# Kernel tuning notes

Hardware: AMD Instinct MI355X
Metric: run time of the kernel (lower is better)

The kernel has to match this reference:

```python
import jax, jax.numpy as jnp
import numpy as np

DIM = 512
HIDDEN = 512
HEADS = 8
HEAD_DIM = HIDDEN // HEADS
SCALE = HEAD_DIM ** -0.5
B, H, W = 2, 64, 64


def setup_inputs() -> dict:
    key = jax.random.key(0)
    ks = jax.random.split(key, 12)
    init = lambda k, shp: jax.random.normal(k, shp, dtype=jnp.float32) * 0.02
    return {
        "x": jax.random.normal(ks[0], (B, DIM, H, W), dtype=jnp.float32),
        "context": jax.random.normal(ks[1], (B, DIM, H, W), dtype=jnp.float32),
        # weights stored [in, out] so y = x @ W + b
        "Wi": init(ks[2], (DIM, HIDDEN)), "bi": jnp.zeros((HIDDEN,), jnp.float32),
        "Wc": init(ks[3], (DIM, HIDDEN)), "bc": jnp.zeros((HIDDEN,), jnp.float32),
        "Wq": init(ks[4], (HIDDEN, HIDDEN)),
        "Wk": init(ks[5], (HIDDEN, HIDDEN)),
        "Wv": init(ks[6], (HIDDEN, HIDDEN)),
        "Wo1": init(ks[7], (HIDDEN, HIDDEN)), "bo1": jnp.zeros((HIDDEN,), jnp.float32),
        "Wo2": init(ks[8], (HIDDEN, DIM)), "bo2": jnp.zeros((DIM,), jnp.float32),
    }


def reference(x, context, Wi, bi, Wc, bc, Wq, Wk, Wv, Wo1, bo1, Wo2, bo2):
    b, c, h, w = x.shape
    s = h * w
    x_seq = x.reshape(b, c, s).transpose(0, 2, 1)        # [B,S,C]
    ctx_seq = context.reshape(b, c, s).transpose(0, 2, 1)

    x_proj = x_seq @ Wi + bi                              # [B,S,Hid]
    ctx_proj = ctx_seq @ Wc + bc

    q = (x_proj @ Wq).reshape(b, s, HEADS, HEAD_DIM)      # [B,S,h,d]
    k = (ctx_proj @ Wk).reshape(b, s, HEADS, HEAD_DIM)
    v = (ctx_proj @ Wv).reshape(b, s, HEADS, HEAD_DIM)

    attn = jnp.einsum('bqhd,bkhd->bhqk', q, k) * SCALE    # [B,h,S,S]
    attn = jax.nn.softmax(attn, axis=-1)
    out = jnp.einsum('bhqk,bkhd->bqhd', attn, v).reshape(b, s, HIDDEN)

    out = jax.nn.gelu(out @ Wo1 + bo1, approximate=False) @ Wo2 + bo2  # [B,S,C]
    return out.transpose(0, 2, 1).reshape(b, c, h, w)
```

## Files before the change

kernel.cpp:

```cpp
#include <hip/hip_runtime.h>

#define SEQ 4096
#define CDIM 512
#define HID 512
#define NB 2
#define NHEADS 8

typedef float f32x4 __attribute__((ext_vector_type(4)));
typedef short bf16x8 __attribute__((ext_vector_type(8)));

static __device__ __forceinline__ short f2bf(float f) {
  unsigned u = __float_as_uint(f);
  u = (u + 0x7fffu + ((u >> 16) & 1u)) >> 16;
  return (short)u;
}
static __device__ __forceinline__ float bf2f(short h) {
  return __uint_as_float(((unsigned)(unsigned short)h) << 16);
}
static __device__ __forceinline__ unsigned pk2bf(float a, float b) {
  unsigned r;
  asm("v_cvt_pk_bf16_f32 %0, %1, %2" : "=v"(r) : "v"(a), "v"(b));
  return r;
}
typedef const __attribute__((address_space(1))) char gas_char;
typedef __attribute__((address_space(3))) char las_char;
static __device__ __forceinline__ void gll16(const char* g, char* l) {
  __builtin_amdgcn_global_load_lds((gas_char*)g, (las_char*)l, 16, 0, 0);
}

__global__ __launch_bounds__(256) void prep_w(
    const float* Wi, const float* Wc, const float* Wq, const float* Wk,
    const float* Wv, const float* Wo1, const float* Wo2,
    unsigned short* wth, unsigned short* wtl) {
  __shared__ float tile[32][33];
  const int z = blockIdx.z;
  const float* src;
  float scale = 1.0f;
  switch (z) {
    case 0: src = Wi; break;
    case 1: src = Wc; break;
    case 2: src = Wq; scale = 0.18033688011112042f; break;
    case 3: src = Wk; break;
    case 4: src = Wv; break;
    case 5: src = Wo1; break;
    default: src = Wo2; break;
  }
  const int n0 = blockIdx.x * 32, k0 = blockIdx.y * 32;
  const int tx = threadIdx.x, ty = threadIdx.y;
  for (int i = ty; i < 32; i += 8)
    tile[i][tx] = src[(k0 + i) * 512 + n0 + tx];
  __syncthreads();
  unsigned short* oh = wth + z * 262144;
  unsigned short* ol = wtl + z * 262144;
  if (z < 2) {
    for (int i = ty; i < 32; i += 8) {
      const float v = tile[i][tx];
      const short h = f2bf(v);
      oh[(k0 + i) * 512 + n0 + tx] = (unsigned short)h;
      ol[(k0 + i) * 512 + n0 + tx] = (unsigned short)f2bf(v - bf2f(h));
    }
  } else {
    for (int i = ty; i < 32; i += 8) {
      const float v = tile[tx][i] * scale;
      const short h = f2bf(v);
      oh[(n0 + i) * 512 + k0 + tx] = (unsigned short)h;
      ol[(n0 + i) * 512 + k0 + tx] = (unsigned short)f2bf(v - bf2f(h));
    }
  }
}

__global__ __launch_bounds__(512) void prep_bias(
    const float* __restrict__ bi, const float* __restrict__ Wq,
    const float* __restrict__ bc, const float* __restrict__ Wk,
    const float* __restrict__ Wv, float* __restrict__ bout) {
  const int z = blockIdx.x;
  const int n = threadIdx.x;
  const float* b = (z == 0) ? bi : bc;
  const float* W = (z == 0) ? Wq : (z == 1) ? Wk : Wv;
  const float s = (z == 0) ? 0.18033688011112042f : 1.0f;
  float acc = 0.0f;
  for (int k = 0; k < 512; ++k) acc += b[k] * W[k * 512 + n];
  bout[z * 512 + n] = acc * s;
}

__global__ __launch_bounds__(256) void prep_x2(
    const float* __restrict__ x, const float* __restrict__ ctx,
    unsigned short* __restrict__ oh0, unsigned short* __restrict__ ol0,
    unsigned short* __restrict__ oh1, unsigned short* __restrict__ ol1) {
  __shared__ float tile[32][33];
  const int b = blockIdx.z & 1;
  const int ten = blockIdx.z >> 1;
  const float* in = ten ? ctx : x;
  unsigned short* oh = ten ? oh1 : oh0;
  unsigned short* ol = ten ? ol1 : ol0;
  const int s0 = blockIdx.x * 32, c0 = blockIdx.y * 32;
  const int tx = threadIdx.x, ty = threadIdx.y;
  const float* ib = in + (long)b * CDIM * SEQ;
  for (int i = ty; i < 32; i += 8)
    tile[i][tx] = ib[(long)(c0 + i) * SEQ + s0 + tx];
  __syncthreads();
  const long ob = (long)b * SEQ * CDIM;
  for (int i = ty; i < 32; i += 8) {
    const float v = tile[tx][i];
    const short h = f2bf(v);
    oh[ob + (long)(s0 + i) * CDIM + c0 + tx] = (unsigned short)h;
    ol[ob + (long)(s0 + i) * CDIM + c0 + tx] = (unsigned short)f2bf(v - bf2f(h));
  }
}

#define OUT_DUAL 0
#define OUT_HI 1
#define OUT_F32 2

struct GemmJob {
  const unsigned short *Ah, *Al, *Wh, *Wl;
  const float* bias;
  void *outA, *outB;
  int tstore;
};

template <int OMODE, bool DO_GELU, bool HASB, int NJOBS, int GY, int NBATCH>
__global__ __launch_bounds__(256) void gemmN(GemmJob J0, GemmJob J1, GemmJob J2) {
  __shared__ __align__(16) char lds[49152];
  const int orig = blockIdx.x + ((blockIdx.y + blockIdx.z * GY) << 3);
  const int total = 8 * GY * NBATCH * NJOBS;
  const int work = (orig & 7) * (total >> 3) + (orig >> 3);
  const int bx = work & 7;
  const int rest = work >> 3;
  const int by = rest % GY;
  const int z = rest / GY;
  const int jz = z / NBATCH;
  const int bz = z % NBATCH;
  const GemmJob J = (NJOBS >= 3 && jz == 2) ? J2 : ((NJOBS >= 2 && jz == 1) ? J1 : J0);
  const int TS = J.tstore;
  const int t = threadIdx.x;
  const int lane = t & 63, wave = t >> 6;
  const int l15 = lane & 15, g = lane >> 4;
  const int m0 = by * 128, n0 = bx * 64;
  const long abase = (long)bz * SEQ * 512;

  const int grow = lane >> 3;
  const int ch = (((lane & 7) << 4) ^ (grow << 4));
  const int chp = ch & 63;
  const char* pa = (const char*)((ch < 64) ? J.Ah : J.Al);
  const char* pw = (const char*)((ch < 64) ? J.Wh : J.Wl);
  const char* aG[4];
#pragma unroll
  for (int i = 0; i < 4; ++i)
    aG[i] = pa + ((abase + (long)(m0 + wave * 32 + i * 8 + grow) * 512) << 1) + chp;
  const char* wG[2];
#pragma unroll
  for (int i = 0; i < 2; ++i)
    wG[i] = pw + (((long)(n0 + wave * 16 + i * 8 + grow) * 512) << 1) + chp;

  f32x4 acc[4][2];
#pragma unroll
  for (int p = 0; p < 4; ++p)
#pragma unroll
    for (int q = 0; q < 2; ++q) acc[p][q] = (f32x4){0.f, 0.f, 0.f, 0.f};

  {
    char* LA = lds;
    char* LW = lds + 16384;
#pragma unroll
    for (int i = 0; i < 4; ++i) gll16(aG[i], LA + wave * 4096 + i * 1024);
#pragma unroll
    for (int i = 0; i < 2; ++i) gll16(wG[i], LW + wave * 2048 + i * 1024);
  }

  int buf = 0;
  for (int k0 = 0; k0 < 512; k0 += 32) {
    char* LA = lds + buf * 24576;
    char* LW = LA + 16384;
    __syncthreads();
    if (k0 + 32 < 512) {
      char* NA = lds + (buf ^ 1) * 24576;
      char* NW = NA + 16384;
      const int koff = (k0 + 32) * 2;
#pragma unroll
      for (int i = 0; i < 4; ++i) gll16(aG[i] + koff, NA + wave * 4096 + i * 1024);
#pragma unroll
      for (int i = 0; i < 2; ++i) gll16(wG[i] + koff, NW + wave * 2048 + i * 1024);
    }

    if (!TS) {
      bf16x8 fbh[2], fbl[2];
#pragma unroll
      for (int q = 0; q < 2; ++q) {
        const int r = wave * 32 + q * 16 + l15;
        const char* rp = LA + r * 128;
        const int sw = (r & 7) << 4;
        fbh[q] = *(const bf16x8*)(rp + ((g << 4) ^ sw));
        fbl[q] = *(const bf16x8*)(rp + (((4 + g) << 4) ^ sw));
      }
#pragma unroll
      for (int p = 0; p < 4; ++p) {
        const int r = p * 16 + l15;
        const char* rp = LW + r * 128;
        const int sw = (r & 7) << 4;
        const bf16x8 fah = *(const bf16x8*)(rp + ((g << 4) ^ sw));
        const bf16x8 fal = *(const bf16x8*)(rp + (((4 + g) << 4) ^ sw));
#pragma unroll
        for (int q = 0; q < 2; ++q) {
          acc[p][q] = __builtin_amdgcn_mfma_f32_16x16x32_bf16(fah, fbh[q], acc[p][q], 0, 0, 0);
          acc[p][q] = __builtin_amdgcn_mfma_f32_16x16x32_bf16(fah, fbl[q], acc[p][q], 0, 0, 0);
          acc[p][q] = __builtin_amdgcn_mfma_f32_16x16x32_bf16(fal, fbh[q], acc[p][q], 0, 0, 0);
        }
      }
    } else {
      const int mB = (wave >> 1) * 64, nB = (wave & 1) * 32;
      bf16x8 fbh[2], fbl[2];
#pragma unroll
      for (int q = 0; q < 2; ++q) {
        const int r = nB + q * 16 + l15;
        const char* rp = LW + r * 128;
        const int sw = (r & 7) << 4;
        fbh[q] = *(const bf16x8*)(rp + ((g << 4) ^ sw));
        fbl[q] = *(const bf16x8*)(rp + (((4 + g) << 4) ^ sw));
      }
#pragma unroll
      for (int p = 0; p < 4; ++p) {
        const int r = mB + p * 16 + l15;
        const char* rp = LA + r * 128;
        const int sw = (r & 7) << 4;
        const bf16x8 fah = *(const bf16x8*)(rp + ((g << 4) ^ sw));
        const bf16x8 fal = *(const bf16x8*)(rp + (((4 + g) << 4) ^ sw));
#pragma unroll
        for (int q = 0; q < 2; ++q) {
          acc[p][q] = __builtin_amdgcn_mfma_f32_16x16x32_bf16(fah, fbh[q], acc[p][q], 0, 0, 0);
          acc[p][q] = __builtin_amdgcn_mfma_f32_16x16x32_bf16(fah, fbl[q], acc[p][q], 0, 0, 0);
          acc[p][q] = __builtin_amdgcn_mfma_f32_16x16x32_bf16(fal, fbh[q], acc[p][q], 0, 0, 0);
        }
      }
    }
    buf ^= 1;
  }

  const long obase = (long)bz * 512 * SEQ;
#pragma unroll
  for (int p = 0; p < 4; ++p)
#pragma unroll
    for (int q = 0; q < 2; ++q) {
      f32x4 v = acc[p][q];
      if (TS) {
        const int m = m0 + (wave >> 1) * 64 + p * 16 + 4 * g;
        const int n = n0 + (wave & 1) * 32 + q * 16 + l15;
        if (HASB) {
          const float b = J.bias[n];
          v[0] += b; v[1] += b; v[2] += b; v[3] += b;
        }
        if (OMODE == OUT_F32) {
          float4 f;
          f.x = v[0]; f.y = v[1]; f.z = v[2]; f.w = v[3];
          *(float4*)((float*)J.outA + obase + (long)n * SEQ + m) = f;
        } else {
          const short4 h4 = make_short4(f2bf(v[0]), f2bf(v[1]), f2bf(v[2]), f2bf(v[3]));
          *(short4*)((unsigned short*)J.outA + obase + (long)n * SEQ + m) = h4;
        }
      } else {
        const int n = n0 + p * 16 + 4 * g;
        const int m = m0 + wave * 32 + q * 16 + l15;
        if (HASB) v += *(const f32x4*)(J.bias + n);
        if (DO_GELU) {
#pragma unroll
          for (int r = 0; r < 4; ++r)
            v[r] = 0.5f * v[r] * (1.0f + erff(v[r] * 0.7071067811865476f));
        }
        unsigned short* oA = (unsigned short*)J.outA + obase + (long)m * 512 + n;
        if (OMODE == OUT_DUAL) {
          short h[4], l[4];
#pragma unroll
          for (int r = 0; r < 4; ++r) {
            h[r] = f2bf(v[r]);
            l[r] = f2bf(v[r] - bf2f(h[r]));
          }
          *(short4*)oA = make_short4(h[0], h[1], h[2], h[3]);
          *(short4*)((unsigned short*)J.outB + obase + (long)m * 512 + n) =
              make_short4(l[0], l[1], l[2], l[3]);
        } else {
          *(short4*)oA = make_short4(f2bf(v[0]), f2bf(v[1]), f2bf(v[2]), f2bf(v[3]));
        }
      }
    }
}

__global__ __launch_bounds__(512) void attn_mfma(
    const unsigned short* __restrict__ qh, const unsigned short* __restrict__ kh,
    const unsigned short* __restrict__ vt, unsigned short* __restrict__ oh,
    unsigned short* __restrict__ ol) {
  __shared__ __align__(16) char smem[32768];
  const int t = threadIdx.x;
  const int lane = t & 63;
  const int wave = t >> 6;
  const int l15 = lane & 15;
  const int g = lane >> 4;
  const int orig = blockIdx.x + ((blockIdx.y + (blockIdx.z << 3)) << 4);
  const int work = ((orig & 7) << 5) + (orig >> 3);
  const int hd = (work >> 4) & 7;
  const int bz = work >> 7;
  const int q0 = (work & 15) * 256;
  const long sbase = (long)bz * SEQ * 512;
  const long tbase = (long)bz * 512 * SEQ;

  const int grow = lane >> 3;
  const int ch = (((lane & 7) << 4) ^ (grow << 4));
  const char* kG = (const char*)kh + (sbase << 1) + hd * 128 +
                   (long)(wave * 8 + grow) * 1024 + ch;
  const char* vG = (const char*)vt +
                   ((tbase + (long)(hd * 64 + wave * 8 + grow) * 4096) << 1) + ch;

  const int swzl = (l15 & 7) << 4;
  const int kfb = l15 * 128 + g * 16;
  const int vfb = l15 * 128 + g * 8;

  bf16x8 qf[2][2];
#pragma unroll
  for (int u = 0; u < 2; ++u) {
    const unsigned short* qrow =
        qh + sbase + (long)(q0 + wave * 32 + u * 16 + l15) * 512 + hd * 64 + g * 8;
    qf[u][0] = *(const bf16x8*)(qrow);
    qf[u][1] = *(const bf16x8*)(qrow + 32);
  }

  bf16x8 vones;
#pragma unroll
  for (int e = 0; e < 8; ++e) vones[e] = (l15 == 0) ? (short)0x3f80 : (short)0;

  f32x4 acc[2][4];
  f32x4 acc5[2];
#pragma unroll
  for (int u = 0; u < 2; ++u) {
    acc5[u] = (f32x4){0.f, 0.f, 0.f, 0.f};
#pragma unroll
    for (int dt = 0; dt < 4; ++dt) acc[u][dt] = (f32x4){0.f, 0.f, 0.f, 0.f};
  }

  gll16(kG, smem + wave * 1024);
  gll16(vG, smem + 8192 + wave * 1024);

  int buf = 0;
  for (int j0 = 0; j0 < SEQ; j0 += 64) {
    char* Kl = smem + buf * 16384;
    char* Vl = Kl + 8192;
    __syncthreads();
    if (j0 + 64 < SEQ) {
      char* Kn = smem + (buf ^ 1) * 16384;
      gll16(kG + (long)(j0 + 64) * 1024, Kn + wave * 1024);
      gll16(vG + (long)(j0 + 64) * 2, Kn + 8192 + wave * 1024);
    }

    f32x4 st[2][4];
    __builtin_amdgcn_s_setprio(1);
#pragma unroll
    for (int kt = 0; kt < 4; ++kt) {
      const bf16x8 ka0 = *(const bf16x8*)(Kl + ((kt * 2048 + kfb) ^ swzl));
      const bf16x8 ka1 = *(const bf16x8*)(Kl + ((kt * 2048 + kfb + 64) ^ swzl));
      f32x4 s0 = {0.f, 0.f, 0.f, 0.f};
      f32x4 s1 = {0.f, 0.f, 0.f, 0.f};
      s0 = __builtin_amdgcn_mfma_f32_16x16x32_bf16(ka0, qf[0][0], s0, 0, 0, 0);
      s0 = __builtin_amdgcn_mfma_f32_16x16x32_bf16(ka1, qf[0][1], s0, 0, 0, 0);
      s1 = __builtin_amdgcn_mfma_f32_16x16x32_bf16(ka0, qf[1][0], s1, 0, 0, 0);
      s1 = __builtin_amdgcn_mfma_f32_16x16x32_bf16(ka1, qf[1][1], s1, 0, 0, 0);
      st[0][kt] = s0;
      st[1][kt] = s1;
    }
    __builtin_amdgcn_s_setprio(0);

    union Pb { bf16x8 v8; unsigned u4[4]; } pb[2][2];
#pragma unroll
    for (int u = 0; u < 2; ++u) {
#pragma unroll
      for (int kt = 0; kt < 4; ++kt)
#pragma unroll
        for (int r = 0; r < 4; ++r)
          st[u][kt][r] = __builtin_amdgcn_exp2f(st[u][kt][r]);
#pragma unroll
      for (int kc = 0; kc < 2; ++kc)
#pragma unroll
        for (int h = 0; h < 2; ++h) {
          pb[u][kc].u4[h * 2 + 0] = pk2bf(st[u][2 * kc + h][0], st[u][2 * kc + h][1]);
          pb[u][kc].u4[h * 2 + 1] = pk2bf(st[u][2 * kc + h][2], st[u][2 * kc + h][3]);
        }
    }

    __builtin_amdgcn_s_setprio(1);
#pragma unroll
    for (int dt = 0; dt < 4; ++dt) {
      union { bf16x8 v8; int2 h2[2]; } va0, va1;
      va0.h2[0] = *(const int2*)(Vl + ((dt * 2048 + vfb) ^ swzl));
      va0.h2[1] = *(const int2*)(Vl + ((dt * 2048 + vfb + 32) ^ swzl));
      va1.h2[0] = *(const int2*)(Vl + ((dt * 2048 + vfb + 64) ^ swzl));
      va1.h2[1] = *(const int2*)(Vl + ((dt * 2048 + vfb + 96) ^ swzl));
      acc[0][dt] = __builtin_amdgcn_mfma_f32_16x16x32_bf16(va0.v8, pb[0][0].v8, acc[0][dt], 0, 0, 0);
      acc[0][dt] = __builtin_amdgcn_mfma_f32_16x16x32_bf16(va1.v8, pb[0][1].v8, acc[0][dt], 0, 0, 0);
      acc[1][dt] = __builtin_amdgcn_mfma_f32_16x16x32_bf16(va0.v8, pb[1][0].v8, acc[1][dt], 0, 0, 0);
      acc[1][dt] = __builtin_amdgcn_mfma_f32_16x16x32_bf16(va1.v8, pb[1][1].v8, acc[1][dt], 0, 0, 0);
    }
#pragma unroll
    for (int u = 0; u < 2; ++u) {
      acc5[u] = __builtin_amdgcn_mfma_f32_16x16x32_bf16(vones, pb[u][0].v8, acc5[u], 0, 0, 0);
      acc5[u] = __builtin_amdgcn_mfma_f32_16x16x32_bf16(vones, pb[u][1].v8, acc5[u], 0, 0, 0);
    }
    __builtin_amdgcn_s_setprio(0);
    buf ^= 1;
  }

#pragma unroll
  for (int u = 0; u < 2; ++u) {
    const float lt = __shfl(acc5[u][0], l15);
    const float inv = 1.0f / lt;
    const long orow = sbase + (long)(q0 + wave * 32 + u * 16 + l15) * 512 + hd * 64;
#pragma unroll
    for (int dt = 0; dt < 4; ++dt) {
      short h[4], l[4];
#pragma unroll
      for (int r = 0; r < 4; ++r) {
        const float v = acc[u][dt][r] * inv;
        h[r] = f2bf(v);
        l[r] = f2bf(v - bf2f(h[r]));
      }
      *(short4*)(oh + orow + dt * 16 + g * 4) = make_short4(h[0], h[1], h[2], h[3]);
      *(short4*)(ol + orow + dt * 16 + g * 4) = make_short4(l[0], l[1], l[2], l[3]);
    }
  }
}

extern "C" void kernel_launch(void* const* d_in, const int* in_sizes, int n_in,
                              void* d_out, int out_size, void* d_ws,
                              size_t ws_size, hipStream_t stream) {
  const float* x   = (const float*)d_in[0];
  const float* ctx = (const float*)d_in[1];
  const float* Wi  = (const float*)d_in[2];
  const float* bi  = (const float*)d_in[3];
  const float* Wc  = (const float*)d_in[4];
  const float* bc  = (const float*)d_in[5];
  const float* Wq  = (const float*)d_in[6];
  const float* Wk  = (const float*)d_in[7];
  const float* Wv  = (const float*)d_in[8];
  const float* Wo1 = (const float*)d_in[9];
  const float* bo1 = (const float*)d_in[10];
  const float* Wo2 = (const float*)d_in[11];
  const float* bo2 = (const float*)d_in[12];
  float* out = (float*)d_out;

  const size_t WP = 262144;
  char* p = (char*)d_ws;
  unsigned short* wth = (unsigned short*)p; p += (size_t)7 * WP * 2;
  unsigned short* wtl = (unsigned short*)p; p += (size_t)7 * WP * 2;
  unsigned short* cwh = (unsigned short*)p; p += (size_t)3 * WP * 2;
  unsigned short* cwl = (unsigned short*)p; p += (size_t)3 * WP * 2;
  float* bqkv = (float*)p; p += 3 * 512 * 4;
  const size_t PLE = (size_t)NB * SEQ * 512;
  unsigned short* P1 = (unsigned short*)p; p += PLE * 2;
  unsigned short* P2 = (unsigned short*)p; p += PLE * 2;
  unsigned short* P3 = (unsigned short*)p; p += PLE * 2;
  unsigned short* P4 = (unsigned short*)p; p += PLE * 2;
  unsigned short* P5 = (unsigned short*)p; p += PLE * 2;
  unsigned short* P6 = (unsigned short*)p; p += PLE * 2;
  unsigned short* P7 = (unsigned short*)d_out;

  const dim3 gb(256);
  const dim3 pg(16, 16, 7), pbk(32, 8);
  const dim3 xg(128, 16, 2 * NB);
  GemmJob jn = {};

  prep_w<<<pg, pbk, 0, stream>>>(Wi, Wc, Wq, Wk, Wv, Wo1, Wo2, wth, wtl);
  prep_bias<<<dim3(3), dim3(512), 0, stream>>>(bi, Wq, bc, Wk, Wv, bqkv);
  prep_x2<<<xg, pbk, 0, stream>>>(x, ctx, P1, P2, P3, P4);
  {
    GemmJob ja = {wth + 2 * WP, wtl + 2 * WP, wth + 0 * WP, wtl + 0 * WP,
                  nullptr, cwh + 0 * WP, cwl + 0 * WP, 0};
    GemmJob jb = {wth + 3 * WP, wtl + 3 * WP, wth + 1 * WP, wtl + 1 * WP,
                  nullptr, cwh + 1 * WP, cwl + 1 * WP, 0};
    GemmJob jc = {wth + 4 * WP, wtl + 4 * WP, wth + 1 * WP, wtl + 1 * WP,
                  nullptr, cwh + 2 * WP, cwl + 2 * WP, 0};
    gemmN<OUT_DUAL, false, false, 3, 4, 1><<<dim3(8, 4, 3), gb, 0, stream>>>(ja, jb, jc);
  }
  {
    GemmJob ja = {P1, P2, cwh + 0 * WP, cwl + 0 * WP, bqkv + 0, P5, nullptr, 0};
    GemmJob jb = {P3, P4, cwh + 1 * WP, cwl + 1 * WP, bqkv + 512, P6, nullptr, 0};
    GemmJob jc = {P3, P4, cwh + 2 * WP, cwl + 2 * WP, bqkv + 1024, P7, nullptr, 1};
    gemmN<OUT_HI, false, true, 3, 32, 2><<<dim3(8, 32, 6), gb, 0, stream>>>(ja, jb, jc);
  }
  attn_mfma<<<dim3(SEQ / 256, NHEADS, NB), dim3(512), 0, stream>>>(P5, P6, P7, P1, P2);
  {
    GemmJob j = {P1, P2, wth + 5 * WP, wtl + 5 * WP, bo1, P3, P4, 0};
    gemmN<OUT_DUAL, true, true, 1, 32, 2><<<dim3(8, 32, 2), gb, 0, stream>>>(j, jn, jn);
  }
  {
    GemmJob j = {P3, P4, wth + 6 * WP, wtl + 6 * WP, bo2, out, nullptr, 1};
    gemmN<OUT_F32, false, true, 1, 32, 2><<<dim3(8, 32, 2), gb, 0, stream>>>(j, jn, jn);
  }
}
```

Before: 214.9 us.

## Triple-buffer GEMM and attention loads and drop a split-bf16 term for QKV

Measured after the change: 218.4 us. No clear change (+1.6%).

```diff
diff --git a/kernel.cpp b/kernel.cpp
--- a/kernel.cpp
+++ b/kernel.cpp
@@ -26,6 +26,11 @@
 typedef __attribute__((address_space(3))) char las_char;
 static __device__ __forceinline__ void gll16(const char* g, char* l) {
   __builtin_amdgcn_global_load_lds((gas_char*)g, (las_char*)l, 16, 0, 0);
+}
+#define WAITV(N) asm volatile("s_waitcnt vmcnt(" #N ")" ::: "memory")
+static __device__ __forceinline__ void pipe_barrier() {
+  __builtin_amdgcn_s_barrier();
+  __builtin_amdgcn_sched_barrier(0);
 }
 
 __global__ __launch_bounds__(256) void prep_w(
@@ -119,9 +124,9 @@
   int tstore;
 };
 
-template <int OMODE, bool DO_GELU, bool HASB, int NJOBS, int GY, int NBATCH>
+template <int OMODE, bool DO_GELU, bool HASB, int NJOBS, int GY, int NBATCH, int TERMS>
 __global__ __launch_bounds__(256) void gemmN(GemmJob J0, GemmJob J1, GemmJob J2) {
-  __shared__ __align__(16) char lds[49152];
+  __shared__ __align__(16) char lds[73728];
   const int orig = blockIdx.x + ((blockIdx.y + blockIdx.z * GY) << 3);
   const int total = 8 * GY * NBATCH * NJOBS;
   const int work = (orig & 7) * (total >> 3) + (orig >> 3);
@@ -153,35 +158,32 @@
   for (int i = 0; i < 2; ++i)
     wG[i] = pw + (((long)(n0 + wave * 16 + i * 8 + grow) * 512) << 1) + chp;
 
+  auto stage = [&](int tt, int b) {
+    char* LA = lds + b * 24576;
+    char* LW = LA + 16384;
+    const int koff = tt * 64;
+#pragma unroll
+    for (int i = 0; i < 4; ++i) gll16(aG[i] + koff, LA + wave * 4096 + i * 1024);
+    gll16(wG[0] + koff, LW + wave * 2048);
+    gll16(wG[1] + koff, LW + wave * 2048 + 1024);
+  };
+
   f32x4 acc[4][2];
 #pragma unroll
   for (int p = 0; p < 4; ++p)
 #pragma unroll
     for (int q = 0; q < 2; ++q) acc[p][q] = (f32x4){0.f, 0.f, 0.f, 0.f};
 
-  {
-    char* LA = lds;
-    char* LW = lds + 16384;
-#pragma unroll
-    for (int i = 0; i < 4; ++i) gll16(aG[i], LA + wave * 4096 + i * 1024);
-#pragma unroll
-    for (int i = 0; i < 2; ++i) gll16(wG[i], LW + wave * 2048 + i * 1024);
-  }
-
-  int buf = 0;
-  for (int k0 = 0; k0 < 512; k0 += 32) {
-    char* LA = lds + buf * 24576;
+  stage(0, 0);
+  stage(1, 1);
+
+  int it = 0;
+  for (int k0 = 0; k0 < 512; k0 += 32, ++it) {
+    if (k0 == 480) { WAITV(0); } else { WAITV(6); }
+    pipe_barrier();
+    if (k0 + 64 < 512) stage(it + 2, (it + 2) % 3);
+    char* LA = lds + (it % 3) * 24576;
     char* LW = LA + 16384;
-    __syncthreads();
-    if (k0 + 32 < 512) {
-      char* NA = lds + (buf ^ 1) * 24576;
-      char* NW = NA + 16384;
-      const int koff = (k0 + 32) * 2;
-#pragma unroll
-      for (int i = 0; i < 4; ++i) gll16(aG[i] + koff, NA + wave * 4096 + i * 1024);
-#pragma unroll
-      for (int i = 0; i < 2; ++i) gll16(wG[i] + koff, NW + wave * 2048 + i * 1024);
-    }
 
     if (!TS) {
       bf16x8 fbh[2], fbl[2];
@@ -199,12 +201,16 @@
         const char* rp = LW + r * 128;
         const int sw = (r & 7) << 4;
         const bf16x8 fah = *(const bf16x8*)(rp + ((g << 4) ^ sw));
-        const bf16x8 fal = *(const bf16x8*)(rp + (((4 + g) << 4) ^ sw));
 #pragma unroll
         for (int q = 0; q < 2; ++q) {
           acc[p][q] = __builtin_amdgcn_mfma_f32_16x16x32_bf16(fah, fbh[q], acc[p][q], 0, 0, 0);
           acc[p][q] = __builtin_amdgcn_mfma_f32_16x16x32_bf16(fah, fbl[q], acc[p][q], 0, 0, 0);
-          acc[p][q] = __builtin_amdgcn_mfma_f32_16x16x32_bf16(fal, fbh[q], acc[p][q], 0, 0, 0);
+        }
+        if (TERMS == 3) {
+          const bf16x8 fal = *(const bf16x8*)(rp + (((4 + g) << 4) ^ sw));
+#pragma unroll
+          for (int q = 0; q < 2; ++q)
+            acc[p][q] = __builtin_amdgcn_mfma_f32_16x16x32_bf16(fal, fbh[q], acc[p][q], 0, 0, 0);
         }
       }
     } else {
@@ -216,7 +222,7 @@
         const char* rp = LW + r * 128;
         const int sw = (r & 7) << 4;
         fbh[q] = *(const bf16x8*)(rp + ((g << 4) ^ sw));
-        fbl[q] = *(const bf16x8*)(rp + (((4 + g) << 4) ^ sw));
+        if (TERMS == 3) fbl[q] = *(const bf16x8*)(rp + (((4 + g) << 4) ^ sw));
       }
 #pragma unroll
       for (int p = 0; p < 4; ++p) {
@@ -228,12 +234,12 @@
 #pragma unroll
         for (int q = 0; q < 2; ++q) {
           acc[p][q] = __builtin_amdgcn_mfma_f32_16x16x32_bf16(fah, fbh[q], acc[p][q], 0, 0, 0);
-          acc[p][q] = __builtin_amdgcn_mfma_f32_16x16x32_bf16(fah, fbl[q], acc[p][q], 0, 0, 0);
+          if (TERMS == 3)
+            acc[p][q] = __builtin_amdgcn_mfma_f32_16x16x32_bf16(fah, fbl[q], acc[p][q], 0, 0, 0);
           acc[p][q] = __builtin_amdgcn_mfma_f32_16x16x32_bf16(fal, fbh[q], acc[p][q], 0, 0, 0);
         }
       }
     }
-    buf ^= 1;
   }
 
   const long obase = (long)bz * 512 * SEQ;
@@ -288,7 +294,7 @@
     const unsigned short* __restrict__ qh, const unsigned short* __restrict__ kh,
     const unsigned short* __restrict__ vt, unsigned short* __restrict__ oh,
     unsigned short* __restrict__ ol) {
-  __shared__ __align__(16) char smem[32768];
+  __shared__ __align__(16) char smem[49152];
   const int t = threadIdx.x;
   const int lane = t & 63;
   const int wave = t >> 6;
@@ -326,6 +332,12 @@
 #pragma unroll
   for (int e = 0; e < 8; ++e) vones[e] = (l15 == 0) ? (short)0x3f80 : (short)0;
 
+  auto stage = [&](int j0s, int b) {
+    char* Kn = smem + b * 16384;
+    gll16(kG + (long)j0s * 1024, Kn + wave * 1024);
+    gll16(vG + (long)j0s * 2, Kn + 8192 + wave * 1024);
+  };
+
   f32x4 acc[2][4];
   f32x4 acc5[2];
 #pragma unroll
@@ -335,19 +347,16 @@
     for (int dt = 0; dt < 4; ++dt) acc[u][dt] = (f32x4){0.f, 0.f, 0.f, 0.f};
   }
 
-  gll16(kG, smem + wave * 1024);
-  gll16(vG, smem + 8192 + wave * 1024);
-
-  int buf = 0;
-  for (int j0 = 0; j0 < SEQ; j0 += 64) {
-    char* Kl = smem + buf * 16384;
+  stage(0, 0);
+  stage(64, 1);
+
+  int it = 0;
+  for (int j0 = 0; j0 < SEQ; j0 += 64, ++it) {
+    if (j0 == SEQ - 64) { WAITV(0); } else { WAITV(2); }
+    pipe_barrier();
+    if (j0 + 128 < SEQ) stage(j0 + 128, (it + 2) % 3);
+    char* Kl = smem + (it % 3) * 16384;
     char* Vl = Kl + 8192;
-    __syncthreads();
-    if (j0 + 64 < SEQ) {
-      char* Kn = smem + (buf ^ 1) * 16384;
-      gll16(kG + (long)(j0 + 64) * 1024, Kn + wave * 1024);
-      gll16(vG + (long)(j0 + 64) * 2, Kn + 8192 + wave * 1024);
-    }
 
     f32x4 st[2][4];
     __builtin_amdgcn_s_setprio(1);
@@ -402,7 +411,6 @@
       acc5[u] = __builtin_amdgcn_mfma_f32_16x16x32_bf16(vones, pb[u][1].v8, acc5[u], 0, 0, 0);
     }
     __builtin_amdgcn_s_setprio(0);
-    buf ^= 1;
   }
 
 #pragma unroll
@@ -474,21 +482,21 @@
                   nullptr, cwh + 1 * WP, cwl + 1 * WP, 0};
     GemmJob jc = {wth + 4 * WP, wtl + 4 * WP, wth + 1 * WP, wtl + 1 * WP,
                   nullptr, cwh + 2 * WP, cwl + 2 * WP, 0};
-    gemmN<OUT_DUAL, false, false, 3, 4, 1><<<dim3(8, 4, 3), gb, 0, stream>>>(ja, jb, jc);
+    gemmN<OUT_DUAL, false, false, 3, 4, 1, 3><<<dim3(8, 4, 3), gb, 0, stream>>>(ja, jb, jc);
   }
   {
     GemmJob ja = {P1, P2, cwh + 0 * WP, cwl + 0 * WP, bqkv + 0, P5, nullptr, 0};
     GemmJob jb = {P3, P4, cwh + 1 * WP, cwl + 1 * WP, bqkv + 512, P6, nullptr, 0};
     GemmJob jc = {P3, P4, cwh + 2 * WP, cwl + 2 * WP, bqkv + 1024, P7, nullptr, 1};
-    gemmN<OUT_HI, false, true, 3, 32, 2><<<dim3(8, 32, 6), gb, 0, stream>>>(ja, jb, jc);
+    gemmN<OUT_HI, false, true, 3, 32, 2, 2><<<dim3(8, 32, 6), gb, 0, stream>>>(ja, jb, jc);
   }
   attn_mfma<<<dim3(SEQ / 256, NHEADS, NB), dim3(512), 0, stream>>>(P5, P6, P7, P1, P2);
   {
     GemmJob j = {P1, P2, wth + 5 * WP, wtl + 5 * WP, bo1, P3, P4, 0};
-    gemmN<OUT_DUAL, true, true, 1, 32, 2><<<dim3(8, 32, 2), gb, 0, stream>>>(j, jn, jn);
+    gemmN<OUT_DUAL, true, true, 1, 32, 2, 3><<<dim3(8, 32, 2), gb, 0, stream>>>(j, jn, jn);
   }
   {
     GemmJob j = {P3, P4, wth + 6 * WP, wtl + 6 * WP, bo2, out, nullptr, 1};
-    gemmN<OUT_F32, false, true, 1, 32, 2><<<dim3(8, 32, 2), gb, 0, stream>>>(j, jn, jn);
-  }
-}
+    gemmN<OUT_F32, false, true, 1, 32, 2, 3><<<dim3(8, 32, 2), gb, 0, stream>>>(j, jn, jn);
+  }
+}
```

## Merge prep kernels into one launch and drop third split-bf16 term in big GEMMs

Applied to the files above, without the earlier changes.

Result: slower. 242.3 us (+12.7%).

```diff
diff --git a/kernel.cpp b/kernel.cpp
--- a/kernel.cpp
+++ b/kernel.cpp
@@ -28,83 +28,85 @@
   __builtin_amdgcn_global_load_lds((gas_char*)g, (las_char*)l, 16, 0, 0);
 }
 
-__global__ __launch_bounds__(256) void prep_w(
+__global__ __launch_bounds__(256) void prep_all(
+    const float* __restrict__ x, const float* __restrict__ ctx,
     const float* Wi, const float* Wc, const float* Wq, const float* Wk,
     const float* Wv, const float* Wo1, const float* Wo2,
-    unsigned short* wth, unsigned short* wtl) {
+    const float* bi, const float* bc,
+    unsigned short* wth, unsigned short* wtl,
+    unsigned short* xh, unsigned short* xl,
+    unsigned short* chh, unsigned short* cll, float* bqkv) {
   __shared__ float tile[32][33];
-  const int z = blockIdx.z;
-  const float* src;
-  float scale = 1.0f;
-  switch (z) {
-    case 0: src = Wi; break;
-    case 1: src = Wc; break;
-    case 2: src = Wq; scale = 0.18033688011112042f; break;
-    case 3: src = Wk; break;
-    case 4: src = Wv; break;
-    case 5: src = Wo1; break;
-    default: src = Wo2; break;
-  }
-  const int n0 = blockIdx.x * 32, k0 = blockIdx.y * 32;
   const int tx = threadIdx.x, ty = threadIdx.y;
-  for (int i = ty; i < 32; i += 8)
-    tile[i][tx] = src[(k0 + i) * 512 + n0 + tx];
-  __syncthreads();
-  unsigned short* oh = wth + z * 262144;
-  unsigned short* ol = wtl + z * 262144;
-  if (z < 2) {
+  const int zz = blockIdx.z;
+  if (zz < 4) {
+    const int b = zz & 1, ten = zz >> 1;
+    const float* in = ten ? ctx : x;
+    unsigned short* oh = ten ? chh : xh;
+    unsigned short* ol = ten ? cll : xl;
+    const int s0 = blockIdx.x * 32, c0 = blockIdx.y * 32;
+    const float* ib = in + (long)b * CDIM * SEQ;
+    for (int i = ty; i < 32; i += 8)
+      tile[i][tx] = ib[(long)(c0 + i) * SEQ + s0 + tx];
+    __syncthreads();
+    const long ob = (long)b * SEQ * CDIM;
     for (int i = ty; i < 32; i += 8) {
-      const float v = tile[i][tx];
+      const float v = tile[tx][i];
       const short h = f2bf(v);
-      oh[(k0 + i) * 512 + n0 + tx] = (unsigned short)h;
-      ol[(k0 + i) * 512 + n0 + tx] = (unsigned short)f2bf(v - bf2f(h));
-    }
-  } else {
-    for (int i = ty; i < 32; i += 8) {
-      const float v = tile[tx][i] * scale;
-      const short h = f2bf(v);
-      oh[(n0 + i) * 512 + k0 + tx] = (unsigned short)h;
-      ol[(n0 + i) * 512 + k0 + tx] = (unsigned short)f2bf(v - bf2f(h));
-    }
-  }
-}
-
-__global__ __launch_bounds__(512) void prep_bias(
-    const float* __restrict__ bi, const float* __restrict__ Wq,
-    const float* __restrict__ bc, const float* __restrict__ Wk,
-    const float* __restrict__ Wv, float* __restrict__ bout) {
-  const int z = blockIdx.x;
-  const int n = threadIdx.x;
-  const float* b = (z == 0) ? bi : bc;
-  const float* W = (z == 0) ? Wq : (z == 1) ? Wk : Wv;
-  const float s = (z == 0) ? 0.18033688011112042f : 1.0f;
-  float acc = 0.0f;
-  for (int k = 0; k < 512; ++k) acc += b[k] * W[k * 512 + n];
-  bout[z * 512 + n] = acc * s;
-}
-
-__global__ __launch_bounds__(256) void prep_x2(
-    const float* __restrict__ x, const float* __restrict__ ctx,
-    unsigned short* __restrict__ oh0, unsigned short* __restrict__ ol0,
-    unsigned short* __restrict__ oh1, unsigned short* __restrict__ ol1) {
-  __shared__ float tile[32][33];
-  const int b = blockIdx.z & 1;
-  const int ten = blockIdx.z >> 1;
-  const float* in = ten ? ctx : x;
-  unsigned short* oh = ten ? oh1 : oh0;
-  unsigned short* ol = ten ? ol1 : ol0;
-  const int s0 = blockIdx.x * 32, c0 = blockIdx.y * 32;
-  const int tx = threadIdx.x, ty = threadIdx.y;
-  const float* ib = in + (long)b * CDIM * SEQ;
-  for (int i = ty; i < 32; i += 8)
-    tile[i][tx] = ib[(long)(c0 + i) * SEQ + s0 + tx];
-  __syncthreads();
-  const long ob = (long)b * SEQ * CDIM;
-  for (int i = ty; i < 32; i += 8) {
-    const float v = tile[tx][i];
-    const short h = f2bf(v);
-    oh[ob + (long)(s0 + i) * CDIM + c0 + tx] = (unsigned short)h;
-    ol[ob + (long)(s0 + i) * CDIM + c0 + tx] = (unsigned short)f2bf(v - bf2f(h));
+      oh[ob + (long)(s0 + i) * CDIM + c0 + tx] = (unsigned short)h;
+      ol[ob + (long)(s0 + i) * CDIM + c0 + tx] = (unsigned short)f2bf(v - bf2f(h));
+    }
+    return;
+  }
+  const int id = blockIdx.x + (blockIdx.y << 7);
+  if (id < 1792) {
+    const int z = id >> 8;
+    const int tl = id & 255;
+    const int n0 = (tl & 15) * 32, k0 = (tl >> 4) * 32;
+    const float* src;
+    float scale = 1.0f;
+    switch (z) {
+      case 0: src = Wi; break;
+      case 1: src = Wc; break;
+      case 2: src = Wq; scale = 0.18033688011112042f; break;
+      case 3: src = Wk; break;
+      case 4: src = Wv; break;
+      case 5: src = Wo1; break;
+      default: src = Wo2; break;
+    }
+    for (int i = ty; i < 32; i += 8)
+      tile[i][tx] = src[(k0 + i) * 512 + n0 + tx];
+    __syncthreads();
+    unsigned short* oh = wth + z * 262144;
+    unsigned short* ol = wtl + z * 262144;
+    if (z < 2) {
+      for (int i = ty; i < 32; i += 8) {
+        const float v = tile[i][tx];
+        const short h = f2bf(v);
+        oh[(k0 + i) * 512 + n0 + tx] = (unsigned short)h;
+        ol[(k0 + i) * 512 + n0 + tx] = (unsigned short)f2bf(v - bf2f(h));
+      }
+    } else {
+      for (int i = ty; i < 32; i += 8) {
+        const float v = tile[tx][i] * scale;
+        const short h = f2bf(v);
+        oh[(n0 + i) * 512 + k0 + tx] = (unsigned short)h;
+        ol[(n0 + i) * 512 + k0 + tx] = (unsigned short)f2bf(v - bf2f(h));
+      }
+    }
+    return;
+  }
+  if (id < 1795) {
+    const int z = id - 1792;
+    const int t = tx + ty * 32;
+    const float* b = (z == 0) ? bi : bc;
+    const float* W = (z == 0) ? Wq : (z == 1) ? Wk : Wv;
+    const float s = (z == 0) ? 0.18033688011112042f : 1.0f;
+    for (int nn = t; nn < 512; nn += 256) {
+      float acc = 0.0f;
+      for (int k = 0; k < 512; ++k) acc += b[k] * W[k * 512 + nn];
+      bqkv[z * 512 + nn] = acc * s;
+    }
   }
 }
 
@@ -119,7 +121,7 @@
   int tstore;
 };
 
-template <int OMODE, bool DO_GELU, bool HASB, int NJOBS, int GY, int NBATCH>
+template <int OMODE, bool DO_GELU, bool HASB, int NJOBS, int GY, int NBATCH, int TERMS>
 __global__ __launch_bounds__(256) void gemmN(GemmJob J0, GemmJob J1, GemmJob J2) {
   __shared__ __align__(16) char lds[49152];
   const int orig = blockIdx.x + ((blockIdx.y + blockIdx.z * GY) << 3);
@@ -199,12 +201,16 @@
         const char* rp = LW + r * 128;
         const int sw = (r & 7) << 4;
         const bf16x8 fah = *(const bf16x8*)(rp + ((g << 4) ^ sw));
-        const bf16x8 fal = *(const bf16x8*)(rp + (((4 + g) << 4) ^ sw));
 #pragma unroll
         for (int q = 0; q < 2; ++q) {
           acc[p][q] = __builtin_amdgcn_mfma_f32_16x16x32_bf16(fah, fbh[q], acc[p][q], 0, 0, 0);
           acc[p][q] = __builtin_amdgcn_mfma_f32_16x16x32_bf16(fah, fbl[q], acc[p][q], 0, 0, 0);
-          acc[p][q] = __builtin_amdgcn_mfma_f32_16x16x32_bf16(fal, fbh[q], acc[p][q], 0, 0, 0);
+        }
+        if (TERMS == 3) {
+          const bf16x8 fal = *(const bf16x8*)(rp + (((4 + g) << 4) ^ sw));
+#pragma unroll
+          for (int q = 0; q < 2; ++q)
+            acc[p][q] = __builtin_amdgcn_mfma_f32_16x16x32_bf16(fal, fbh[q], acc[p][q], 0, 0, 0);
         }
       }
     } else {
@@ -216,7 +222,7 @@
         const char* rp = LW + r * 128;
         const int sw = (r & 7) << 4;
         fbh[q] = *(const bf16x8*)(rp + ((g << 4) ^ sw));
-        fbl[q] = *(const bf16x8*)(rp + (((4 + g) << 4) ^ sw));
+        if (TERMS == 3) fbl[q] = *(const bf16x8*)(rp + (((4 + g) << 4) ^ sw));
       }
 #pragma unroll
       for (int p = 0; p < 4; ++p) {
@@ -228,7 +234,8 @@
 #pragma unroll
         for (int q = 0; q < 2; ++q) {
           acc[p][q] = __builtin_amdgcn_mfma_f32_16x16x32_bf16(fah, fbh[q], acc[p][q], 0, 0, 0);
-          acc[p][q] = __builtin_amdgcn_mfma_f32_16x16x32_bf16(fah, fbl[q], acc[p][q], 0, 0, 0);
+          if (TERMS == 3)
+            acc[p][q] = __builtin_amdgcn_mfma_f32_16x16x32_bf16(fah, fbl[q], acc[p][q], 0, 0, 0);
           acc[p][q] = __builtin_amdgcn_mfma_f32_16x16x32_bf16(fal, fbh[q], acc[p][q], 0, 0, 0);
         }
       }
@@ -460,13 +467,11 @@
   unsigned short* P7 = (unsigned short*)d_out;
 
   const dim3 gb(256);
-  const dim3 pg(16, 16, 7), pbk(32, 8);
-  const dim3 xg(128, 16, 2 * NB);
   GemmJob jn = {};
 
-  prep_w<<<pg, pbk, 0, stream>>>(Wi, Wc, Wq, Wk, Wv, Wo1, Wo2, wth, wtl);
-  prep_bias<<<dim3(3), dim3(512), 0, stream>>>(bi, Wq, bc, Wk, Wv, bqkv);
-  prep_x2<<<xg, pbk, 0, stream>>>(x, ctx, P1, P2, P3, P4);
+  prep_all<<<dim3(128, 16, 5), dim3(32, 8), 0, stream>>>(
+      x, ctx, Wi, Wc, Wq, Wk, Wv, Wo1, Wo2, bi, bc,
+      wth, wtl, P1, P2, P3, P4, bqkv);
   {
     GemmJob ja = {wth + 2 * WP, wtl + 2 * WP, wth + 0 * WP, wtl + 0 * WP,
                   nullptr, cwh + 0 * WP, cwl + 0 * WP, 0};
@@ -474,21 +479,21 @@
                   nullptr, cwh + 1 * WP, cwl + 1 * WP, 0};
     GemmJob jc = {wth + 4 * WP, wtl + 4 * WP, wth + 1 * WP, wtl + 1 * WP,
                   nullptr, cwh + 2 * WP, cwl + 2 * WP, 0};
-    gemmN<OUT_DUAL, false, false, 3, 4, 1><<<dim3(8, 4, 3), gb, 0, stream>>>(ja, jb, jc);
+    gemmN<OUT_DUAL, false, false, 3, 4, 1, 3><<<dim3(8, 4, 3), gb, 0, stream>>>(ja, jb, jc);
   }
   {
     GemmJob ja = {P1, P2, cwh + 0 * WP, cwl + 0 * WP, bqkv + 0, P5, nullptr, 0};
     GemmJob jb = {P3, P4, cwh + 1 * WP, cwl + 1 * WP, bqkv + 512, P6, nullptr, 0};
     GemmJob jc = {P3, P4, cwh + 2 * WP, cwl + 2 * WP, bqkv + 1024, P7, nullptr, 1};
-    gemmN<OUT_HI, false, true, 3, 32, 2><<<dim3(8, 32, 6), gb, 0, stream>>>(ja, jb, jc);
+    gemmN<OUT_HI, false, true, 3, 32, 2, 2><<<dim3(8, 32, 6), gb, 0, stream>>>(ja, jb, jc);
   }
   attn_mfma<<<dim3(SEQ / 256, NHEADS, NB), dim3(512), 0, stream>>>(P5, P6, P7, P1, P2);
   {
     GemmJob j = {P1, P2, wth + 5 * WP, wtl + 5 * WP, bo1, P3, P4, 0};
-    gemmN<OUT_DUAL, true, true, 1, 32, 2><<<dim3(8, 32, 2), gb, 0, stream>>>(j, jn, jn);
+    gemmN<OUT_DUAL, true, true, 1, 32, 2, 2><<<dim3(8, 32, 2), gb, 0, stream>>>(j, jn, jn);
   }
   {
     GemmJob j = {P3, P4, wth + 6 * WP, wtl + 6 * WP, bo2, out, nullptr, 1};
-    gemmN<OUT_F32, false, true, 1, 32, 2><<<dim3(8, 32, 2), gb, 0, stream>>>(j, jn, jn);
-  }
-}
+    gemmN<OUT_F32, false, true, 1, 32, 2, 2><<<dim3(8, 32, 2), gb, 0, stream>>>(j, jn, jn);
+  }
+}
```
